# Kernel optimization log

Hardware: AMD Instinct MI355X
Metric: run time of the kernel (lower is better)

## Reference

```python
import jax, jax.numpy as jnp
import numpy as np

DIM = 1024
HEADS = 16
HEAD_DIM = DIM // HEADS
HIDDEN = 4 * DIM
EPS = 1e-5


def layer_norm(x, g, b):
    mu = jnp.mean(x, axis=-1, keepdims=True)
    var = jnp.mean(jnp.square(x - mu), axis=-1, keepdims=True)
    return (x - mu) * jax.lax.rsqrt(var + EPS) * g + b


def fast_gelu(x):
    # Ascend fast_gelu == x * sigmoid(1.702 * x)
    return x * jax.nn.sigmoid(1.702 * x)


def setup_inputs() -> dict:
    key = jax.random.key(0)
    ks = jax.random.split(key, 12)
    B, N, C = 16, 577, DIM
    s_in = 1.0 / np.sqrt(DIM)
    s_hid = 1.0 / np.sqrt(HIDDEN)
    return {
        "x": jax.random.normal(ks[0], (B * N, C), jnp.float32),
        "norm1_g": jnp.ones((C,), jnp.float32),
        "norm1_b": jnp.zeros((C,), jnp.float32),
        "Wq": jax.random.normal(ks[1], (C, C), jnp.float32) * s_in,
        "Wk": jax.random.normal(ks[2], (C, C), jnp.float32) * s_in,
        "Wv": jax.random.normal(ks[3], (C, C), jnp.float32) * s_in,
        "Wp": jax.random.normal(ks[4], (C, C), jnp.float32) * s_in,
        "bp": jnp.zeros((C,), jnp.float32),
        "norm2_g": jnp.ones((C,), jnp.float32),
        "norm2_b": jnp.zeros((C,), jnp.float32),
        "W1": jax.random.normal(ks[5], (HIDDEN, C), jnp.float32) * s_in,
        "b1": jnp.zeros((HIDDEN,), jnp.float32),
        "W2": jax.random.normal(ks[6], (C, HIDDEN), jnp.float32) * s_hid,
        "b2": jnp.zeros((C,), jnp.float32),
        "B": B,
        "N": N,
        "C": C,
    }


def reference(x, norm1_g, norm1_b, Wq, Wk, Wv, Wp, bp, norm2_g, norm2_b, W1, b1, W2, b2, B, N, C):
    scale = HEAD_DIM ** -0.5

    h = layer_norm(x, norm1_g, norm1_b)          # [B*N, C]
    # qkv projections (qkv_bias=False), reshape to [B, H, N, D]
    def split_heads(y):
        return y.reshape(B, N, HEADS, HEAD_DIM).transpose(0, 2, 1, 3)

    q = split_heads(h @ Wq.T)
    k = split_heads(h @ Wk.T)
    v = split_heads(h @ Wv.T)

    attn = jnp.einsum('bhqd,bhkd->bhqk', q, k) * scale
    attn = jax.nn.softmax(attn, axis=-1)
    o = jnp.einsum('bhqk,bhkd->bhqd', attn, v)   # [B, H, N, D]
    o = o.transpose(0, 2, 1, 3).reshape(B * N, C)
    y = o @ Wp.T + bp                            # attention output proj

    x = x + y                                    # residual 1 (drop_path=0)
    h2 = layer_norm(x, norm2_g, norm2_b)
    m = fast_gelu(h2 @ W1.T + b1) @ W2.T + b2    # MLP (drop=0)
    return x + m                                 # residual 2
```

## Files before the change

kernel.cpp:

```cpp
#include <hip/hip_runtime.h>

typedef short  short8  __attribute__((ext_vector_type(8)));
typedef float  float4v __attribute__((ext_vector_type(4)));

#define DIM      1024
#define HEADS    16
#define HEAD_DIM 64
#define HIDDEN   4096
#define BATCH    16
#define SEQ      577
#define M_ROWS   (BATCH*SEQ)
#define NPAD2    640
#define QKVLD    3072
#define LOG2E    1.4426950408889634f

static __device__ __forceinline__ unsigned short f2bf(float f) {
  unsigned int u = __float_as_uint(f);
  u += 0x7FFFu + ((u >> 16) & 1u);
  return (unsigned short)(u >> 16);
}
static __device__ __forceinline__ void gload_lds16(const void* g, void* l) {
  __builtin_amdgcn_global_load_lds(
      (const __attribute__((address_space(1))) void*)g,
      (__attribute__((address_space(3))) void*)l, 16, 0, 0);
}

__global__ __launch_bounds__(256) void convert_all_kernel(
    const float* __restrict__ Wq, const float* __restrict__ Wk,
    const float* __restrict__ Wv, const float* __restrict__ Wp,
    const float* __restrict__ W1, const float* __restrict__ W2,
    unsigned short* __restrict__ wqkv, unsigned short* __restrict__ wp,
    unsigned short* __restrict__ w1, unsigned short* __restrict__ w2) {
  const int S = DIM * DIM / 4;
  int i = blockIdx.x * 256 + threadIdx.x;
  const float* src; unsigned short* dst; int rel;
  if (i < 4 * S) {
    if (i < S)        { src = Wq; dst = wqkv;               rel = i; }
    else if (i < 2*S) { src = Wk; dst = wqkv + DIM * DIM;   rel = i - S; }
    else if (i < 3*S) { src = Wv; dst = wqkv + 2*DIM*DIM;   rel = i - 2*S; }
    else              { src = Wp; dst = wp;                 rel = i - 3*S; }
  } else if (i < 8*S) { src = W1; dst = w1;                 rel = i - 4*S; }
  else                { src = W2; dst = w2;                 rel = i - 8*S; }
  float4 v = ((const float4*)src)[rel];
  union { unsigned short s[4]; uint2 u; } p;
  p.s[0] = f2bf(v.x); p.s[1] = f2bf(v.y); p.s[2] = f2bf(v.z); p.s[3] = f2bf(v.w);
  ((uint2*)dst)[rel] = p.u;
}

__global__ __launch_bounds__(256) void ln_kernel(
    const float* __restrict__ x, const float* __restrict__ g,
    const float* __restrict__ b, unsigned short* __restrict__ out) {
  int row = blockIdx.x, tid = threadIdx.x;
  const float* xr = x + (long long)row * DIM;
  float4 v = *(const float4*)(xr + tid * 4);
  float s1 = v.x + v.y + v.z + v.w;
  float s2 = v.x*v.x + v.y*v.y + v.z*v.z + v.w*v.w;
  #pragma unroll
  for (int o = 32; o; o >>= 1) { s1 += __shfl_xor(s1, o); s2 += __shfl_xor(s2, o); }
  __shared__ float a1[4], a2[4];
  int wid = tid >> 6, lane = tid & 63;
  if (lane == 0) { a1[wid] = s1; a2[wid] = s2; }
  __syncthreads();
  s1 = a1[0] + a1[1] + a1[2] + a1[3];
  s2 = a2[0] + a2[1] + a2[2] + a2[3];
  float mean = s1 * (1.f / DIM);
  float var  = s2 * (1.f / DIM) - mean * mean;
  float rstd = rsqrtf(var + 1e-5f);
  float4 gv = *(const float4*)(g + tid * 4);
  float4 bv = *(const float4*)(b + tid * 4);
  union { unsigned short s[4]; uint2 u; } p;
  p.s[0] = f2bf((v.x - mean) * rstd * gv.x + bv.x);
  p.s[1] = f2bf((v.y - mean) * rstd * gv.y + bv.y);
  p.s[2] = f2bf((v.z - mean) * rstd * gv.z + bv.z);
  p.s[3] = f2bf((v.w - mean) * rstd * gv.w + bv.w);
  *(uint2*)(out + (long long)row * DIM + tid * 4) = p.u;
}

__global__ __launch_bounds__(256) void transpose_v_kernel(
    const unsigned short* __restrict__ v, unsigned short* __restrict__ vt) {
  int nt0 = blockIdx.x * 64;
  int bh = blockIdx.y;
  int b = bh >> 4, h = bh & 15;
  __shared__ unsigned short T[64][72];
  int tid = threadIdx.x;
  int r = tid >> 3;
  int c = tid & 7;
  #pragma unroll
  for (int p = 0; p < 2; p++) {
    int row = p * 32 + r;
    int n = nt0 + row;
    uint4 val = (uint4){0u, 0u, 0u, 0u};
    if (n < SEQ)
      val = *(const uint4*)(v + ((long long)(b * SEQ + n)) * QKVLD + h * HEAD_DIM + c * 8);
    *(uint4*)&T[row][c * 8] = val;
  }
  __syncthreads();
  #pragma unroll
  for (int p = 0; p < 2; p++) {
    int d = p * 32 + (tid >> 3);
    union { unsigned short s[8]; uint4 u; } o;
    #pragma unroll
    for (int i = 0; i < 8; i++) o.s[i] = T[c * 8 + i][d];
    *(uint4*)(vt + ((long long)bh * HEAD_DIM + d) * NPAD2 + nt0 + c * 8) = o.u;
  }
}

template <bool MASK>
static __device__ __forceinline__ void attn_tile(
    const unsigned short* Ks, const unsigned short* Vs, unsigned short* Ps,
    const short8 (&af)[2][2], float4v (&oacc)[2][4], float4v (&sumacc)[2],
    int quad, int l16, int wid) {
  const float CE = 0.125f * LOG2E;

  short8 bfr[4][2];
  #pragma unroll
  for (int j = 0; j < 4; j++) {
    int r = j * 16 + l16;
    #pragma unroll
    for (int ks = 0; ks < 2; ks++)
      bfr[j][ks] = *(const short8*)(Ks + r * 64 + ((ks * 4 + quad) ^ (l16 & 7)) * 8);
  }

  float4v sacc[2][4];
  #pragma unroll
  for (int i = 0; i < 2; i++)
    #pragma unroll
    for (int j = 0; j < 4; j++) sacc[i][j] = (float4v){0.f, 0.f, 0.f, 0.f};
  #pragma unroll
  for (int i = 0; i < 2; i++)
    #pragma unroll
    for (int j = 0; j < 4; j++)
      #pragma unroll
      for (int ks = 0; ks < 2; ks++)
        sacc[i][j] = __builtin_amdgcn_mfma_f32_16x16x32_bf16(af[i][ks], bfr[j][ks], sacc[i][j], 0, 0, 0);

  #pragma unroll
  for (int i = 0; i < 2; i++) {
    #pragma unroll
    for (int reg = 0; reg < 4; reg++) {
      int prow = wid * 32 + i * 16 + quad * 4 + reg;
      #pragma unroll
      for (int j = 0; j < 4; j++) {
        float pv;
        if constexpr (MASK) {
          pv = (j == 0 && l16 == 0) ? __builtin_amdgcn_exp2f(sacc[i][j][reg] * CE) : 0.f;
        } else {
          pv = __builtin_amdgcn_exp2f(sacc[i][j][reg] * CE);
        }
        int pcol = j * 16 + l16;
        Ps[prow * 64 + (((pcol >> 3) ^ (prow & 7)) * 8) + (pcol & 7)] = f2bf(pv);
      }
    }
  }

  short8 paf[2][2], vbf[4][2];
  #pragma unroll
  for (int i = 0; i < 2; i++) {
    int r = wid * 32 + i * 16 + l16;
    #pragma unroll
    for (int kk = 0; kk < 2; kk++)
      paf[i][kk] = *(const short8*)(Ps + r * 64 + ((kk * 4 + quad) ^ (l16 & 7)) * 8);
  }
  #pragma unroll
  for (int j = 0; j < 4; j++) {
    int r = j * 16 + l16;
    #pragma unroll
    for (int kk = 0; kk < 2; kk++)
      vbf[j][kk] = *(const short8*)(Vs + r * 64 + ((kk * 4 + quad) ^ (l16 & 7)) * 8);
  }
  const short ov = (short)0x3F80;
  const short8 ones = (short8){ov, ov, ov, ov, ov, ov, ov, ov};
  #pragma unroll
  for (int i = 0; i < 2; i++) {
    #pragma unroll
    for (int kk = 0; kk < 2; kk++) {
      #pragma unroll
      for (int j = 0; j < 4; j++)
        oacc[i][j] = __builtin_amdgcn_mfma_f32_16x16x32_bf16(paf[i][kk], vbf[j][kk], oacc[i][j], 0, 0, 0);
      sumacc[i] = __builtin_amdgcn_mfma_f32_16x16x32_bf16(paf[i][kk], ones, sumacc[i], 0, 0, 0);
    }
  }
}

__global__ __launch_bounds__(256, 3) void flash_attn_kernel(
    const unsigned short* __restrict__ q,
    const unsigned short* __restrict__ k,
    const unsigned short* __restrict__ vt,
    unsigned short* __restrict__ o) {
  int qt = blockIdx.x;
  int bh = blockIdx.y;
  int b = bh >> 4, h = bh & 15;
  int q0 = qt * 128;
  int tid = threadIdx.x, lane = tid & 63, wid = tid >> 6;
  int quad = lane >> 4, l16 = lane & 15;
  long long rowbase = (long long)b * SEQ;

  __shared__ __align__(16) unsigned short SM[24576];
  unsigned short* Ps = SM + 16384;

  auto stageKV = [&](int sel, int kt) {
    unsigned short* Ks_ = SM + sel * 8192;
    unsigned short* Vs_ = Ks_ + 4096;
    #pragma unroll
    for (int p = 0; p < 2; p++) {
      int r = wid * 16 + p * 8 + (lane >> 3);
      int c = lane & 7;
      int gk = kt * 64 + r; if (gk > SEQ - 1) gk = SEQ - 1;
      gload_lds16(k + (rowbase + gk) * QKVLD + h * HEAD_DIM + ((c ^ (r & 7)) * 8),
                  Ks_ + (wid * 16 + p * 8) * 64);
      gload_lds16(vt + ((long long)bh * HEAD_DIM + r) * NPAD2 + kt * 64 + ((c ^ (r & 7)) * 8),
                  Vs_ + (wid * 16 + p * 8) * 64);
    }
  };

  short8 af[2][2];
  #pragma unroll
  for (int i = 0; i < 2; i++) {
    int gr = q0 + wid * 32 + i * 16 + l16;
    if (gr > SEQ - 1) gr = SEQ - 1;
    const unsigned short* qr = q + (rowbase + gr) * QKVLD + h * HEAD_DIM;
    #pragma unroll
    for (int ks = 0; ks < 2; ks++)
      af[i][ks] = *(const short8*)(qr + (ks * 4 + quad) * 8);
  }

  float4v oacc[2][4];
  float4v sumacc[2];
  #pragma unroll
  for (int i = 0; i < 2; i++) {
    sumacc[i] = (float4v){0.f, 0.f, 0.f, 0.f};
    #pragma unroll
    for (int j = 0; j < 4; j++) oacc[i][j] = (float4v){0.f, 0.f, 0.f, 0.f};
  }

  stageKV(0, 0);
  asm volatile("s_waitcnt vmcnt(0)" ::: "memory");
  __builtin_amdgcn_s_barrier();

  for (int kt = 0; kt < 10; kt++) {
    int cur = kt & 1;
    if (kt < 9) stageKV(cur ^ 1, kt + 1);
    const unsigned short* Ks_ = SM + cur * 8192;
    const unsigned short* Vs_ = Ks_ + 4096;
    if (kt < 9) attn_tile<false>(Ks_, Vs_, Ps, af, oacc, sumacc, quad, l16, wid);
    else        attn_tile<true >(Ks_, Vs_, Ps, af, oacc, sumacc, quad, l16, wid);
    __builtin_amdgcn_sched_barrier(0);
    asm volatile("s_waitcnt vmcnt(0)" ::: "memory");
    __builtin_amdgcn_s_barrier();
  }

  #pragma unroll
  for (int i = 0; i < 2; i++) {
    #pragma unroll
    for (int reg = 0; reg < 4; reg++) {
      int grow = q0 + wid * 32 + i * 16 + quad * 4 + reg;
      if (grow >= SEQ) continue;
      float inv = 1.f / sumacc[i][reg];
      #pragma unroll
      for (int j = 0; j < 4; j++) {
        int d = j * 16 + l16;
        o[(rowbase + grow) * DIM + h * HEAD_DIM + d] = f2bf(oacc[i][j][reg] * inv);
      }
    }
  }
}

enum { EPI_BF16 = 0, EPI_BIAS_RES_F32 = 2, EPI_BIAS_GELU_BF16 = 3 };

template <int EPI>
__global__ __launch_bounds__(256, 2) void gemm_nt(
    const unsigned short* __restrict__ A, int lda,
    const unsigned short* __restrict__ B, int ldb,
    void* __restrict__ Cout, int ldc,
    const float* __restrict__ bias, const float* __restrict__ res,
    int M, int N, int K) {
  int mt = gridDim.x, nt = gridDim.y;
  int id = blockIdx.y * mt + blockIdx.x;
  int band  = id / (8 * nt);
  int rem   = id - band * 8 * nt;
  int mrem  = mt - band * 8;
  int bandh = mrem < 8 ? mrem : 8;
  int lm = rem % bandh;
  int nb = rem / bandh;
  int m0 = (band * 8 + lm) * 128, n0 = nb * 128;

  int tid = threadIdx.x;
  int lane = tid & 63, wid = tid >> 6;
  int wm = wid >> 1, wn = wid & 1;
  int quad = lane >> 4, l16 = lane & 15;

  __shared__ __align__(16) char SMEM[65536];

  float4v acc[4][4];
  #pragma unroll
  for (int i = 0; i < 4; i++)
    #pragma unroll
    for (int j = 0; j < 4; j++) acc[i][j] = (float4v){0.f, 0.f, 0.f, 0.f};

  int lr8 = lane >> 3;
  int lc8 = lane & 7;
  int sc  = (lc8 ^ lr8) * 8;

  auto stage = [&](int sel, int k0) {
    unsigned short* As_ = (unsigned short*)SMEM + sel * (2 * 128 * 64);
    unsigned short* Bs_ = As_ + 128 * 64;
    #pragma unroll
    for (int p = 0; p < 4; p++) {
      int ra = wid * 32 + p * 8;
      int gr = m0 + ra + lr8; if (gr > M - 1) gr = M - 1;
      gload_lds16(A + (long long)gr * lda + k0 + sc, As_ + ra * 64);
      int gn = n0 + ra + lr8; if (gn > N - 1) gn = N - 1;
      gload_lds16(B + (long long)gn * ldb + k0 + sc, Bs_ + ra * 64);
    }
  };

  int T = K >> 6;
  stage(0, 0);
  asm volatile("s_waitcnt vmcnt(0)" ::: "memory");
  __builtin_amdgcn_s_barrier();

  for (int t = 0; t < T; t++) {
    int cur = t & 1;
    if (t + 1 < T) stage(cur ^ 1, (t + 1) << 6);
    const unsigned short* As_ = (const unsigned short*)SMEM + cur * (2 * 128 * 64);
    const unsigned short* Bs_ = As_ + 128 * 64;
    #pragma unroll
    for (int ks = 0; ks < 2; ks++) {
      short8 af[4], bfr[4];
      #pragma unroll
      for (int i = 0; i < 4; i++)
        af[i]  = *(const short8*)(As_ + (wm * 64 + i * 16 + l16) * 64 + (((ks * 4 + quad) ^ (l16 & 7)) * 8));
      #pragma unroll
      for (int j = 0; j < 4; j++)
        bfr[j] = *(const short8*)(Bs_ + (wn * 64 + j * 16 + l16) * 64 + (((ks * 4 + quad) ^ (l16 & 7)) * 8));
      #pragma unroll
      for (int i = 0; i < 4; i++)
        #pragma unroll
        for (int j = 0; j < 4; j++)
          acc[i][j] = __builtin_amdgcn_mfma_f32_16x16x32_bf16(af[i], bfr[j], acc[i][j], 0, 0, 0);
    }
    __builtin_amdgcn_sched_barrier(0);
    asm volatile("s_waitcnt vmcnt(0)" ::: "memory");
    __builtin_amdgcn_s_barrier();
  }

  float* cs = (float*)SMEM + wid * (16 * 68);
  int erow = lane >> 2;
  int eq   = lane & 3;

  #pragma unroll
  for (int i = 0; i < 4; i++) {
    #pragma unroll
    for (int j = 0; j < 4; j++)
      #pragma unroll
      for (int r = 0; r < 4; r++)
        cs[(quad * 4 + r) * 68 + j * 16 + l16] = acc[i][j][r];
    int grow = m0 + wm * 64 + i * 16 + erow;
    bool rowok = grow < M;

    if constexpr (EPI == EPI_BIAS_RES_F32) {
      #pragma unroll
      for (int t = 0; t < 4; t++) {
        int colb = t * 16 + eq * 4;
        int gcol = n0 + wn * 64 + colb;
        if (!rowok || gcol >= N) continue;
        float4 vv = *(const float4*)&cs[erow * 68 + colb];
        float4 bb = *(const float4*)&bias[gcol];
        const float4 rr = *(const float4*)&res[(long long)grow * ldc + gcol];
        vv.x += bb.x + rr.x; vv.y += bb.y + rr.y;
        vv.z += bb.z + rr.z; vv.w += bb.w + rr.w;
        *(float4*)((float*)Cout + (long long)grow * ldc + gcol) = vv;
      }
    } else {
      #pragma unroll
      for (int h = 0; h < 2; h++) {
        int colb = h * 32 + eq * 8;
        int gcol = n0 + wn * 64 + colb;
        if (!rowok || gcol >= N) continue;
        float4 a0 = *(const float4*)&cs[erow * 68 + colb];
        float4 a1 = *(const float4*)&cs[erow * 68 + colb + 4];
        float vs[8] = {a0.x, a0.y, a0.z, a0.w, a1.x, a1.y, a1.z, a1.w};
        if constexpr (EPI == EPI_BIAS_GELU_BF16) {
          float4 b0 = *(const float4*)&bias[gcol];
          float4 b1 = *(const float4*)&bias[gcol + 4];
          float bs[8] = {b0.x, b0.y, b0.z, b0.w, b1.x, b1.y, b1.z, b1.w};
          #pragma unroll
          for (int e = 0; e < 8; e++) {
            float tt = vs[e] + bs[e];
            float ex = __builtin_amdgcn_exp2f(tt * -2.4554669595930156f);
            vs[e] = tt / (1.f + ex);
          }
        }
        union { unsigned short s[8]; uint4 u; } p;
        #pragma unroll
        for (int e = 0; e < 8; e++) p.s[e] = f2bf(vs[e]);
        *(uint4*)((unsigned short*)Cout + (long long)grow * ldc + gcol) = p.u;
      }
    }
  }
}

extern "C" void kernel_launch(void* const* d_in, const int* in_sizes, int n_in,
                              void* d_out, int out_size, void* d_ws, size_t ws_size,
                              hipStream_t stream) {
  const float* x   = (const float*)d_in[0];
  const float* g1  = (const float*)d_in[1];
  const float* be1 = (const float*)d_in[2];
  const float* Wq  = (const float*)d_in[3];
  const float* Wk  = (const float*)d_in[4];
  const float* Wv  = (const float*)d_in[5];
  const float* Wp  = (const float*)d_in[6];
  const float* bp  = (const float*)d_in[7];
  const float* g2  = (const float*)d_in[8];
  const float* be2 = (const float*)d_in[9];
  const float* W1  = (const float*)d_in[10];
  const float* b1  = (const float*)d_in[11];
  const float* W2  = (const float*)d_in[12];
  const float* b2  = (const float*)d_in[13];
  float* out = (float*)d_out;

  char* ws = (char*)d_ws;
  size_t off = 0;
  auto alloc = [&](size_t bytes) {
    size_t r = off; off += (bytes + 255) & ~(size_t)255; return r;
  };
  unsigned short* wqkv_bf = (unsigned short*)(ws + alloc((size_t)3 * DIM * DIM * 2));
  unsigned short* wp_bf   = (unsigned short*)(ws + alloc((size_t)DIM * DIM * 2));
  unsigned short* w1_bf   = (unsigned short*)(ws + alloc((size_t)HIDDEN * DIM * 2));
  unsigned short* w2_bf   = (unsigned short*)(ws + alloc((size_t)HIDDEN * DIM * 2));
  unsigned short* h_bf    = (unsigned short*)(ws + alloc((size_t)M_ROWS * DIM * 2));
  unsigned short* qkv_bf  = (unsigned short*)(ws + alloc((size_t)M_ROWS * QKVLD * 2));
  unsigned short* vt_bf   = (unsigned short*)(ws + alloc((size_t)256 * HEAD_DIM * NPAD2 * 2));

  unsigned short* o_bf  = h_bf;
  unsigned short* h2_bf = h_bf;
  unsigned short* u_bf  = qkv_bf;
  float*          x1    = out;

  convert_all_kernel<<<12 * (DIM * DIM / 4) / 256, 256, 0, stream>>>(
      Wq, Wk, Wv, Wp, W1, W2, wqkv_bf, wp_bf, w1_bf, w2_bf);

  ln_kernel<<<M_ROWS, 256, 0, stream>>>(x, g1, be1, h_bf);

  gemm_nt<EPI_BF16><<<dim3(73, 24), 256, 0, stream>>>(h_bf, DIM, wqkv_bf, DIM,
      qkv_bf, QKVLD, nullptr, nullptr, M_ROWS, 3 * DIM, DIM);

  transpose_v_kernel<<<dim3(10, 256), 256, 0, stream>>>(qkv_bf + 2 * DIM, vt_bf);

  flash_attn_kernel<<<dim3(5, 256), 256, 0, stream>>>(
      qkv_bf, qkv_bf + DIM, vt_bf, o_bf);

  gemm_nt<EPI_BIAS_RES_F32><<<dim3(73, 8), 256, 0, stream>>>(o_bf, DIM, wp_bf, DIM,
      x1, DIM, bp, x, M_ROWS, DIM, DIM);

  ln_kernel<<<M_ROWS, 256, 0, stream>>>(x1, g2, be2, h2_bf);

  gemm_nt<EPI_BIAS_GELU_BF16><<<dim3(73, 32), 256, 0, stream>>>(h2_bf, DIM, w1_bf, DIM,
      u_bf, HIDDEN, b1, nullptr, M_ROWS, HIDDEN, DIM);

  gemm_nt<EPI_BIAS_RES_F32><<<dim3(73, 8), 256, 0, stream>>>(u_bf, HIDDEN, w2_bf, HIDDEN,
      out, DIM, b2, x1, M_ROWS, DIM, HIDDEN);
}
```

Baseline: 539.5 us.

## Pipeline global-to-LDS loads with partial vmcnt waits and XCD-aware block remap

Changes the double-buffered loops in the attention and GEMM kernels so the next tile's loads are issued before waiting only on the current tile (vmcnt(4)/vmcnt(8)). Loads can then overlap compute instead of being drained at the end of each iteration. It also remaps workgroup IDs so consecutive tiles land on the same XCD for L2 locality, and precomputes load base pointers to cut address arithmetic. The risk is correctness: the partial waits depend on the exact count of outstanding loads, and removing the sched_barrier lets the compiler reorder code.

```diff
diff --git a/kernel.cpp b/kernel.cpp
--- a/kernel.cpp
+++ b/kernel.cpp
@@ -23,6 +23,12 @@
   __builtin_amdgcn_global_load_lds(
       (const __attribute__((address_space(1))) void*)g,
       (__attribute__((address_space(3))) void*)l, 16, 0, 0);
+}
+static __device__ __forceinline__ int xcd_chunk(int w, int nwg) {
+  int xcd = w & 7, rest = w >> 3;
+  int q = nwg >> 3, r = nwg & 7;
+  int base = xcd < r ? xcd * (q + 1) : r * (q + 1) + (xcd - r) * q;
+  return base + rest;
 }
 
 __global__ __launch_bounds__(256) void convert_all_kernel(
@@ -187,8 +193,10 @@
     const unsigned short* __restrict__ k,
     const unsigned short* __restrict__ vt,
     unsigned short* __restrict__ o) {
-  int qt = blockIdx.x;
-  int bh = blockIdx.y;
+  int w = blockIdx.y * 5 + blockIdx.x;
+  int id = xcd_chunk(w, 5 * 256);
+  int qt = id % 5;
+  int bh = id / 5;
   int b = bh >> 4, h = bh & 15;
   int q0 = qt * 128;
   int tid = threadIdx.x, lane = tid & 63, wid = tid >> 6;
@@ -198,19 +206,26 @@
   __shared__ __align__(16) unsigned short SM[24576];
   unsigned short* Ps = SM + 16384;
 
+  int sr = wid * 16 + (lane >> 3);
+  int scc = (lane & 7) ^ (sr & 7);
+  const unsigned short* kbase = k + (rowbase + sr) * QKVLD + h * HEAD_DIM + scc * 8;
+  const unsigned short* kbase2 = k + (rowbase + sr + 8) * QKVLD + h * HEAD_DIM + (((lane & 7) ^ ((sr + 8) & 7)) * 8);
+  const unsigned short* vbase = vt + ((long long)bh * HEAD_DIM + sr) * NPAD2 + scc * 8;
+  const unsigned short* vbase2 = vt + ((long long)bh * HEAD_DIM + sr + 8) * NPAD2 + (((lane & 7) ^ ((sr + 8) & 7)) * 8);
+
   auto stageKV = [&](int sel, int kt) {
     unsigned short* Ks_ = SM + sel * 8192;
     unsigned short* Vs_ = Ks_ + 4096;
-    #pragma unroll
-    for (int p = 0; p < 2; p++) {
-      int r = wid * 16 + p * 8 + (lane >> 3);
-      int c = lane & 7;
-      int gk = kt * 64 + r; if (gk > SEQ - 1) gk = SEQ - 1;
-      gload_lds16(k + (rowbase + gk) * QKVLD + h * HEAD_DIM + ((c ^ (r & 7)) * 8),
-                  Ks_ + (wid * 16 + p * 8) * 64);
-      gload_lds16(vt + ((long long)bh * HEAD_DIM + r) * NPAD2 + kt * 64 + ((c ^ (r & 7)) * 8),
-                  Vs_ + (wid * 16 + p * 8) * 64);
-    }
+    long long koff = (long long)kt * 64 * QKVLD;
+    long long koff2 = koff;
+    if (kt == 9) {
+      koff  -= (long long)((kt * 64 + sr)     - (SEQ - 1) > 0 ? (kt * 64 + sr)     - (SEQ - 1) : 0) * QKVLD;
+      koff2 -= (long long)((kt * 64 + sr + 8) - (SEQ - 1) > 0 ? (kt * 64 + sr + 8) - (SEQ - 1) : 0) * QKVLD;
+    }
+    gload_lds16(kbase  + koff,  Ks_ + sr * 64 - (lane >> 3) * 64);
+    gload_lds16(kbase2 + koff2, Ks_ + (sr + 8) * 64 - (lane >> 3) * 64);
+    gload_lds16(vbase  + kt * 64, Vs_ + sr * 64 - (lane >> 3) * 64);
+    gload_lds16(vbase2 + kt * 64, Vs_ + (sr + 8) * 64 - (lane >> 3) * 64);
   };
 
   short8 af[2][2];
@@ -234,18 +249,21 @@
   }
 
   stageKV(0, 0);
-  asm volatile("s_waitcnt vmcnt(0)" ::: "memory");
-  __builtin_amdgcn_s_barrier();
 
   for (int kt = 0; kt < 10; kt++) {
     int cur = kt & 1;
-    if (kt < 9) stageKV(cur ^ 1, kt + 1);
+    if (kt < 9) {
+      stageKV(cur ^ 1, kt + 1);
+      asm volatile("s_waitcnt vmcnt(4)" ::: "memory");
+    } else {
+      asm volatile("s_waitcnt vmcnt(0)" ::: "memory");
+    }
+    __builtin_amdgcn_s_barrier();
     const unsigned short* Ks_ = SM + cur * 8192;
     const unsigned short* Vs_ = Ks_ + 4096;
     if (kt < 9) attn_tile<false>(Ks_, Vs_, Ps, af, oacc, sumacc, quad, l16, wid);
     else        attn_tile<true >(Ks_, Vs_, Ps, af, oacc, sumacc, quad, l16, wid);
-    __builtin_amdgcn_sched_barrier(0);
-    asm volatile("s_waitcnt vmcnt(0)" ::: "memory");
+    asm volatile("" ::: "memory");
     __builtin_amdgcn_s_barrier();
   }
 
@@ -275,7 +293,8 @@
     const float* __restrict__ bias, const float* __restrict__ res,
     int M, int N, int K) {
   int mt = gridDim.x, nt = gridDim.y;
-  int id = blockIdx.y * mt + blockIdx.x;
+  int nwg = mt * nt;
+  int id = xcd_chunk(blockIdx.y * mt + blockIdx.x, nwg);
   int band  = id / (8 * nt);
   int rem   = id - band * 8 * nt;
   int mrem  = mt - band * 8;
@@ -298,8 +317,18 @@
     for (int j = 0; j < 4; j++) acc[i][j] = (float4v){0.f, 0.f, 0.f, 0.f};
 
   int lr8 = lane >> 3;
-  int lc8 = lane & 7;
-  int sc  = (lc8 ^ lr8) * 8;
+  int sc  = ((lane & 7) ^ lr8) * 8;
+
+  const unsigned short* pA[4];
+  const unsigned short* pB[4];
+  #pragma unroll
+  for (int p = 0; p < 4; p++) {
+    int ra = wid * 32 + p * 8;
+    int gr = m0 + ra + lr8; if (gr > M - 1) gr = M - 1;
+    pA[p] = A + (long long)gr * lda + sc;
+    int gn = n0 + ra + lr8; if (gn > N - 1) gn = N - 1;
+    pB[p] = B + (long long)gn * ldb + sc;
+  }
 
   auto stage = [&](int sel, int k0) {
     unsigned short* As_ = (unsigned short*)SMEM + sel * (2 * 128 * 64);
@@ -307,21 +336,23 @@
     #pragma unroll
     for (int p = 0; p < 4; p++) {
       int ra = wid * 32 + p * 8;
-      int gr = m0 + ra + lr8; if (gr > M - 1) gr = M - 1;
-      gload_lds16(A + (long long)gr * lda + k0 + sc, As_ + ra * 64);
-      int gn = n0 + ra + lr8; if (gn > N - 1) gn = N - 1;
-      gload_lds16(B + (long long)gn * ldb + k0 + sc, Bs_ + ra * 64);
+      gload_lds16(pA[p] + k0, As_ + ra * 64);
+      gload_lds16(pB[p] + k0, Bs_ + ra * 64);
     }
   };
 
   int T = K >> 6;
   stage(0, 0);
-  asm volatile("s_waitcnt vmcnt(0)" ::: "memory");
-  __builtin_amdgcn_s_barrier();
 
   for (int t = 0; t < T; t++) {
     int cur = t & 1;
-    if (t + 1 < T) stage(cur ^ 1, (t + 1) << 6);
+    if (t + 1 < T) {
+      stage(cur ^ 1, (t + 1) << 6);
+      asm volatile("s_waitcnt vmcnt(8)" ::: "memory");
+    } else {
+      asm volatile("s_waitcnt vmcnt(0)" ::: "memory");
+    }
+    __builtin_amdgcn_s_barrier();
     const unsigned short* As_ = (const unsigned short*)SMEM + cur * (2 * 128 * 64);
     const unsigned short* Bs_ = As_ + 128 * 64;
     #pragma unroll
@@ -339,8 +370,7 @@
         for (int j = 0; j < 4; j++)
           acc[i][j] = __builtin_amdgcn_mfma_f32_16x16x32_bf16(af[i], bfr[j], acc[i][j], 0, 0, 0);
     }
-    __builtin_amdgcn_sched_barrier(0);
-    asm volatile("s_waitcnt vmcnt(0)" ::: "memory");
+    asm volatile("" ::: "memory");
     __builtin_amdgcn_s_barrier();
   }
 
```

New measurement: 532.0 us. No clear change (-1.4%).
